# Optimization experiments

Measured on AMD Instinct MI355X. Metric: run time of the kernel, lower is better.

## Reference

```python
import jax, jax.numpy as jnp
import numpy as np

D = 128
N_ATOMS = 200000
E_ATOMS = 800000
G = 2000            # num molecule graphs = nDrug + nProtein
N_BIG = 7000        # nDrug + nProtein + nSe
E_BIG = 200000
N_EMB = 100001


def _edges(key, n, e):
    # random edges guaranteed to have no self-loops (PyG convs strip/re-add them)
    k1, k2 = jax.random.split(key)
    src = jax.random.randint(k1, (e,), 0, n)
    off = jax.random.randint(k2, (e,), 1, n)
    return jnp.stack([src, (src + off) % n])


def setup_inputs() -> dict:
    key = jax.random.key(0)
    ks = jax.random.split(key, 40)
    s = 0.09  # ~1/sqrt(D) init scale
    nrm = lambda i, shape: jax.random.normal(ks[i], shape, dtype=jnp.float32) * s
    inp = {}
    inp['x_ids'] = jax.random.randint(ks[0], (N_BIG,), 0, N_EMB)
    inp['drugEdges'] = _edges(ks[1], N_BIG, E_BIG)
    inp['seEdges'] = _edges(ks[2], 5000, 1000)  # unused by forward
    inp['drugNodes'] = jax.random.randint(ks[3], (1000,), 0, N_BIG)
    inp['seNodes'] = jax.random.randint(ks[4], (5000,), 0, N_BIG)
    inp['proteinNodes'] = jax.random.randint(ks[5], (1000,), 0, N_EMB)
    inp['proteinWeight'] = jax.random.normal(ks[6], (1000,), dtype=jnp.float32)
    inp['atom_x'] = jax.random.randint(ks[7], (N_ATOMS,), 0, N_EMB)
    inp['atom_edge_index'] = _edges(ks[8], N_ATOMS, E_ATOMS)
    inp['atom_batch'] = jnp.sort(jax.random.randint(ks[9], (N_ATOMS,), 0, G))
    inp['nDrug'] = 1000
    inp['emb'] = jax.random.uniform(ks[10], (N_EMB, D), minval=0.001, maxval=0.3, dtype=jnp.float32)
    for i in range(3):
        inp[f'gatW{i+1}'] = nrm(11 + i, (D, D))
        inp[f'attS{i+1}'] = nrm(14 + i, (D,))
        inp[f'attD{i+1}'] = nrm(17 + i, (D,))
        inp[f'gatB{i+1}'] = nrm(20 + i, (D,))
        inp[f'poolP{i+1}'] = nrm(23 + i, (D,))
    inp['lin1_W'] = nrm(26, (2 * D, D))
    inp['lin1_b'] = nrm(27, (D,))
    inp['gcn1_W'] = nrm(28, (D, D))
    inp['gcn1_b'] = nrm(29, (D,))
    inp['gcn2_W'] = nrm(30, (D, D))
    inp['gcn2_b'] = nrm(31, (D,))
    return inp


def _gat(x, src, dst, n, W, a_s, a_d, b):
    # PyG GATConv, 1 head: h = xW; e_ij = LeakyReLU(a_s.h_j + a_d.h_i);
    # softmax over incoming edges of i (self-loops re-added); out_i = sum_j alpha_ij h_j + b
    h = x @ W
    loops = jnp.arange(n)
    s = jnp.concatenate([src, loops])
    d = jnp.concatenate([dst, loops])
    e = jax.nn.leaky_relu((h @ a_s)[s] + (h @ a_d)[d], 0.2)
    m = jax.ops.segment_max(e, d, num_segments=n)
    ex = jnp.exp(e - m[d])
    z = jax.ops.segment_sum(ex, d, num_segments=n)
    w = ex / z[d]
    return jax.ops.segment_sum(w[:, None] * h[s], d, num_segments=n) + b


def _gcn(x, src, dst, n, W, b):
    loops = jnp.arange(n)
    s = jnp.concatenate([src, loops])
    d = jnp.concatenate([dst, loops])
    deg = jax.ops.segment_sum(jnp.ones(d.shape[0], x.dtype), d, num_segments=n)
    dis = deg ** -0.5
    coef = dis[s] * dis[d]
    return jax.ops.segment_sum(coef[:, None] * (x @ W)[s], d, num_segments=n) + b


def _topk1(x, p):
    # TopKPooling with ratio=1: keep all nodes, gate by tanh of projection score
    score = (x @ p) / jnp.linalg.norm(p)
    return x * jnp.tanh(score)[:, None]


def _gmp_gap(x, batch, g):
    mx = jax.ops.segment_max(x, batch, num_segments=g)
    sm = jax.ops.segment_sum(x, batch, num_segments=g)
    cnt = jax.ops.segment_sum(jnp.ones((x.shape[0], 1), x.dtype), batch, num_segments=g)
    return jnp.concatenate([mx, sm / jnp.maximum(cnt, 1.0)], axis=1)


def reference(x_ids, drugEdges, seEdges, drugNodes, seNodes, proteinNodes, proteinWeight,
              atom_x, atom_edge_index, atom_batch, nDrug, emb,
              gatW1, attS1, attD1, gatB1, poolP1,
              gatW2, attS2, attD2, gatB2, poolP2,
              gatW3, attS3, attD3, gatB3, poolP3,
              lin1_W, lin1_b, gcn1_W, gcn1_b, gcn2_W, gcn2_b):
    na = atom_x.shape[0]
    asrc, adst = atom_edge_index[0], atom_edge_index[1]
    xa = emb[atom_x]                                   # [na, D]
    xa = jax.nn.relu(_gat(xa, asrc, adst, na, gatW1, attS1, attD1, gatB1))
    xa = _topk1(xa, poolP1)
    x1 = _gmp_gap(xa, atom_batch, G)                   # [G, 2D]
    xa = jax.nn.relu(_gat(xa, asrc, adst, na, gatW2, attS2, attD2, gatB2))
    xa = _topk1(xa, poolP2)
    x2 = _gmp_gap(xa, atom_batch, G)
    xa = jax.nn.relu(_gat(xa, asrc, adst, na, gatW3, attS3, attD3, gatB3))
    xa = _topk1(xa, poolP3)
    x3 = _gmp_gap(xa, atom_batch, G)
    xDP = jax.nn.relu((x1 + x2 + x3) @ lin1_W + lin1_b)  # [G, D]
    nProtein = proteinNodes.shape[0]
    xse = emb[x_ids[nDrug + nProtein:]]                # side-effect node embeddings
    xb = jnp.concatenate([xDP, xse], axis=0)           # [N_BIG, D]
    dsrc, ddst = drugEdges[0], drugEdges[1]
    xb = jax.nn.relu(_gcn(xb, dsrc, ddst, N_BIG, gcn1_W, gcn1_b))
    xb = jax.nn.relu(_gcn(xb, dsrc, ddst, N_BIG, gcn2_W, gcn2_b))
    return (xb[drugNodes], xb[seNodes], xb)
```

## Files before the change

kernel.cpp:

```cpp
#include <hip/hip_runtime.h>
#include <cfloat>
#include <cmath>

#define D 128
#define N_ATOMS 200000
#define E_ATOMS 800000
#define G_GROUPS 2000
#define N_BIG 7000
#define E_BIG 200000
#define N_ALL (N_ATOMS + N_BIG)
#define E_ALL (E_ATOMS + E_BIG)

static inline int ceil_div(int a, int b) { return (a + b - 1) / b; }

typedef __attribute__((ext_vector_type(8))) short bf16x8;
typedef __attribute__((ext_vector_type(4))) float f32x4;

__device__ inline short f2bf(float f) {
  unsigned u = __builtin_bit_cast(unsigned, f);
  u = (u + 0x7FFF + ((u >> 16) & 1)) >> 16;
  return (short)u;
}
__device__ inline float bf2f(short h) {
  unsigned u = ((unsigned)(unsigned short)h) << 16;
  return __builtin_bit_cast(float, u);
}
__device__ inline float bflo(unsigned p) { return __builtin_bit_cast(float, p << 16); }
__device__ inline float bfhi(unsigned p) { return __builtin_bit_cast(float, p & 0xFFFF0000u); }
__device__ inline unsigned bfpack(float x, float y) {
  return ((unsigned)(unsigned short)f2bf(x)) | (((unsigned)(unsigned short)f2bf(y)) << 16);
}
__device__ inline float leaky(float e) { return fmaxf(e, 0.2f * e); }
__device__ inline float fast_tanh(float x) {
  float cx = fminf(fmaxf(x, -15.f), 15.f);
  float t = __expf(2.f * cx);
  return (t - 1.f) * __frcp_rn(t + 1.f);
}

__global__ void count_all(const int* __restrict__ adst, const int* __restrict__ ddst, int* __restrict__ deg,
                          int* __restrict__ rank) {
  int i = blockIdx.x * 256 + threadIdx.x;
  if (i < E_ATOMS)
    rank[i] = atomicAdd(&deg[adst[i]], 1);
  else if (i < E_ALL)
    rank[i] = atomicAdd(&deg[N_ATOMS + ddst[i - E_ATOMS]], 1);
}

__global__ void fill_csx(const int* __restrict__ asrc, const int* __restrict__ adst,
                         const int* __restrict__ dsrc, const int* __restrict__ ddst,
                         const int* __restrict__ rpx, const int* __restrict__ rank, int* __restrict__ csx) {
  int i = blockIdx.x * 256 + threadIdx.x;
  if (i < E_ATOMS) {
    csx[rpx[adst[i]] + rank[i]] = asrc[i];
  } else if (i < E_ALL) {
    int k = i - E_ATOMS;
    csx[rpx[N_ATOMS + ddst[k]] + rank[i]] = dsrc[k];
  }
}

__global__ void fill_pad(const int* __restrict__ deg, const int* __restrict__ rpx, int* __restrict__ csx) {
  int d = blockIdx.x * 256 + threadIdx.x;
  if (d >= N_ALL) return;
  int dg = deg[d];
  int b = rpx[d], e = rpx[d + 1];
  int sv = (d < N_ATOMS) ? d : d - N_ATOMS;
  for (int j = b + dg; j < e; ++j) csx[j] = sv;
}

__global__ void make_cntp(const int* __restrict__ deg, int* __restrict__ cntp, int n) {
  int i = blockIdx.x * 256 + threadIdx.x;
  if (i < n) cntp[i] = (deg[i] + 8) & ~7;
}

__global__ __launch_bounds__(256) void scan_phase1(const int* __restrict__ in, int* __restrict__ out,
                                                   int* __restrict__ bsums, int n) {
  __shared__ int lds[256];
  int t = threadIdx.x;
  int base = blockIdx.x * 1024;
  int v[4];
  int s = 0;
#pragma unroll
  for (int j = 0; j < 4; ++j) {
    int i = base + t * 4 + j;
    v[j] = (i < n) ? in[i] : 0;
    s += v[j];
  }
  lds[t] = s;
  __syncthreads();
  for (int off = 1; off < 256; off <<= 1) {
    int x = (t >= off) ? lds[t - off] : 0;
    __syncthreads();
    lds[t] += x;
    __syncthreads();
  }
  int excl = lds[t] - s;
  if (t == 255) bsums[blockIdx.x] = lds[255];
  int run = excl;
#pragma unroll
  for (int j = 0; j < 4; ++j) {
    int i = base + t * 4 + j;
    if (i < n) out[i] = run;
    run += v[j];
  }
}

__global__ __launch_bounds__(256) void scan_phase2(int* __restrict__ bsums, int* __restrict__ total_out, int nb) {
  __shared__ int lds[256];
  int t = threadIdx.x;
  int s = (t < nb) ? bsums[t] : 0;
  lds[t] = s;
  __syncthreads();
  for (int off = 1; off < 256; off <<= 1) {
    int x = (t >= off) ? lds[t - off] : 0;
    __syncthreads();
    lds[t] += x;
    __syncthreads();
  }
  if (t < nb) bsums[t] = lds[t] - s;
  if (t == 255) total_out[0] = lds[255];
}

__global__ void scan_phase3(int* __restrict__ out, const int* __restrict__ bsums, int n) {
  int i = blockIdx.x * 256 + threadIdx.x;
  if (i < n) out[i] += bsums[i >> 10];
}

__global__ __launch_bounds__(256) void prep_kernel(const float* __restrict__ W0, const float* __restrict__ W1,
                                                   const float* __restrict__ W2, const float* __restrict__ W3,
                                                   const float* __restrict__ W4, short* __restrict__ Wsplit,
                                                   const float* __restrict__ p0, const float* __restrict__ p1,
                                                   const float* __restrict__ p2, float* __restrict__ pn) {
  int b = blockIdx.x;
  if (b < 5) {
    const float* W = (b == 0) ? W0 : (b == 1) ? W1 : (b == 2) ? W2 : (b == 3) ? W3 : W4;
    short* dstH = Wsplit + (size_t)b * 16384;
    int t = threadIdx.x;
    int col = t & 127;
    int half = t >> 7;
#pragma unroll
    for (int kg = 0; kg < 8; ++kg) {
      int k0 = kg * 16 + half * 8;
      short vh[8];
#pragma unroll
      for (int j = 0; j < 8; ++j) vh[j] = f2bf(W[(k0 + j) * 128 + col]);
      int byte_off = (col * 256 + k0 * 2) ^ ((col & 7) << 4);
      *(bf16x8*)((char*)dstH + byte_off) = *(bf16x8*)vh;
    }
  } else {
    int t = threadIdx.x;
    int g = t >> 6, lane = t & 63;
    if (g < 3) {
      const float* p = (g == 0) ? p0 : (g == 1) ? p1 : p2;
      float2 v = ((const float2*)p)[lane];
      float s = v.x * v.x + v.y * v.y;
#pragma unroll
      for (int off = 32; off; off >>= 1) s += __shfl_xor(s, off);
      if (lane == 0) pn[g] = 1.f / sqrtf(s);
    }
  }
}

__global__ __launch_bounds__(512) void gemm_bf16(const short* __restrict__ A, const short* __restrict__ Wsp,
                                                 short* __restrict__ H, float* __restrict__ hs,
                                                 float* __restrict__ hd, const float* __restrict__ aS,
                                                 const float* __restrict__ aD, int M) {
  __shared__ short Wl[16384];
  int t = threadIdx.x;
  {
    const uint4* src = (const uint4*)Wsp;
    uint4* dst = (uint4*)Wl;
#pragma unroll
    for (int i = 0; i < 4; ++i) dst[t + i * 512] = src[t + i * 512];
  }
  __syncthreads();
  int wave = t >> 6, lane = t & 63;
  int lr = lane & 15, lq = lane >> 4;
  int row0 = blockIdx.x * 256 + wave * 32;
  f32x4 acc[2][8];
#pragma unroll
  for (int rt = 0; rt < 2; ++rt)
#pragma unroll
    for (int ct = 0; ct < 8; ++ct) acc[rt][ct] = (f32x4){0.f, 0.f, 0.f, 0.f};

#pragma unroll
  for (int ks = 0; ks < 4; ++ks) {
    int k8 = ks * 32 + lq * 8;
    bf16x8 Af[2];
#pragma unroll
    for (int rt = 0; rt < 2; ++rt) {
      int row = row0 + rt * 16 + lr;
      if (row < M) {
        Af[rt] = *(const bf16x8*)(A + (size_t)row * D + k8);
      } else {
        Af[rt] = (bf16x8){0, 0, 0, 0, 0, 0, 0, 0};
      }
    }
#pragma unroll
    for (int ct = 0; ct < 8; ++ct) {
      int col = ct * 16 + lr;
      int byte_off = (col * 256 + k8 * 2) ^ ((col & 7) << 4);
      bf16x8 Bh = *(bf16x8*)((char*)Wl + byte_off);
#pragma unroll
      for (int rt = 0; rt < 2; ++rt)
        acc[rt][ct] = __builtin_amdgcn_mfma_f32_16x16x32_bf16(Af[rt], Bh, acc[rt][ct], 0, 0, 0);
    }
  }
#pragma unroll
  for (int rt = 0; rt < 2; ++rt)
#pragma unroll
    for (int ct = 0; ct < 8; ++ct) {
      int col = ct * 16 + lr;
#pragma unroll
      for (int i = 0; i < 4; ++i) {
        int row = row0 + rt * 16 + lq * 4 + i;
        if (row < M) H[(size_t)row * D + col] = f2bf(acc[rt][ct][i]);
      }
    }
  if (aS) {
    float sA[8], sD[8];
#pragma unroll
    for (int ct = 0; ct < 8; ++ct) {
      sA[ct] = aS[ct * 16 + lr];
      sD[ct] = aD[ct * 16 + lr];
    }
#pragma unroll
    for (int rt = 0; rt < 2; ++rt)
#pragma unroll
      for (int i = 0; i < 4; ++i) {
        float ps = 0.f, pd = 0.f;
#pragma unroll
        for (int ct = 0; ct < 8; ++ct) {
          ps = fmaf(acc[rt][ct][i], sA[ct], ps);
          pd = fmaf(acc[rt][ct][i], sD[ct], pd);
        }
#pragma unroll
        for (int off = 1; off < 16; off <<= 1) {
          ps += __shfl_xor(ps, off);
          pd += __shfl_xor(pd, off);
        }
        int row = row0 + rt * 16 + lq * 4 + i;
        if (lr == 0 && row < M) {
          hs[row] = ps;
          hd[row] = pd;
        }
      }
  }
}

__global__ void edge_weights(const float* __restrict__ hs, const float* __restrict__ hd,
                             const int* __restrict__ rpx, const int* __restrict__ deg,
                             const int* __restrict__ csx, float* __restrict__ wts,
                             float* __restrict__ invz, int N) {
  int d = blockIdx.x * 256 + threadIdx.x;
  if (d >= N) return;
  int b = rpx[d];
  int cnt = rpx[d + 1] - b;
  int dg = deg[d];
  float hdd = hd[d];
  float es = leaky(hs[d] + hdd);
  float m = es;
  for (int j = 0; j < dg; ++j) m = fmaxf(m, leaky(hs[csx[b + j]] + hdd));
  float z = 0.f;
  for (int j = 0; j < dg; ++j) {
    float w = __expf(leaky(hs[csx[b + j]] + hdd) - m);
    wts[b + j] = w;
    z += w;
  }
  float wself = __expf(es - m);
  wts[b + dg] = wself;
  z += wself;
  for (int j = dg + 1; j < cnt; ++j) wts[b + j] = 0.f;
  invz[d] = 1.f / z;
}

__global__ void gcn_weights(const int* __restrict__ rpx, const int* __restrict__ deg,
                            const int* __restrict__ csx, const float* __restrict__ dis,
                            float* __restrict__ wtsG, int N) {
  int dl = blockIdx.x * 256 + threadIdx.x;
  if (dl >= N) return;
  int d = N_ATOMS + dl;
  int b = rpx[d];
  int cnt = rpx[d + 1] - b;
  int dg = deg[d];
  float dd = dis[dl];
  for (int j = 0; j < dg; ++j) wtsG[b + j] = dis[csx[b + j]] * dd;
  wtsG[b + dg] = dd * dd;
  for (int j = dg + 1; j < cnt; ++j) wtsG[b + j] = 0.f;
}

__global__ __launch_bounds__(256) void gat_gather(const short* __restrict__ H, const int* __restrict__ rpx,
                                                  const int* __restrict__ csx, const float* __restrict__ wts,
                                                  const float* __restrict__ invz, const float* __restrict__ bias,
                                                  const float* __restrict__ poolP, const float* __restrict__ pnL,
                                                  short* __restrict__ Xout, int N) {
  int wid = (blockIdx.x * 256 + threadIdx.x) >> 6;
  int d = __builtin_amdgcn_readfirstlane(wid);
  if (d >= N) return;
  int lane = threadIdx.x & 63;
  int rb = rpx[d];
  int cnt = rpx[d + 1] - rb;
  const unsigned* H2 = (const unsigned*)H;
  float ax = 0.f, ay = 0.f;
  for (int i = 0; i < cnt; i += 8) {
    int s0 = csx[rb + i + 0], s1 = csx[rb + i + 1], s2 = csx[rb + i + 2], s3 = csx[rb + i + 3];
    int s4 = csx[rb + i + 4], s5 = csx[rb + i + 5], s6 = csx[rb + i + 6], s7 = csx[rb + i + 7];
    float w0 = wts[rb + i + 0], w1 = wts[rb + i + 1], w2 = wts[rb + i + 2], w3 = wts[rb + i + 3];
    float w4 = wts[rb + i + 4], w5 = wts[rb + i + 5], w6 = wts[rb + i + 6], w7 = wts[rb + i + 7];
    unsigned h0 = H2[(size_t)s0 * 64 + lane];
    unsigned h1 = H2[(size_t)s1 * 64 + lane];
    unsigned h2 = H2[(size_t)s2 * 64 + lane];
    unsigned h3 = H2[(size_t)s3 * 64 + lane];
    unsigned h4 = H2[(size_t)s4 * 64 + lane];
    unsigned h5 = H2[(size_t)s5 * 64 + lane];
    unsigned h6 = H2[(size_t)s6 * 64 + lane];
    unsigned h7 = H2[(size_t)s7 * 64 + lane];
    ax = fmaf(w0, bflo(h0), ax);
    ay = fmaf(w0, bfhi(h0), ay);
    ax = fmaf(w1, bflo(h1), ax);
    ay = fmaf(w1, bfhi(h1), ay);
    ax = fmaf(w2, bflo(h2), ax);
    ay = fmaf(w2, bfhi(h2), ay);
    ax = fmaf(w3, bflo(h3), ax);
    ay = fmaf(w3, bfhi(h3), ay);
    ax = fmaf(w4, bflo(h4), ax);
    ay = fmaf(w4, bfhi(h4), ay);
    ax = fmaf(w5, bflo(h5), ax);
    ay = fmaf(w5, bfhi(h5), ay);
    ax = fmaf(w6, bflo(h6), ax);
    ay = fmaf(w6, bfhi(h6), ay);
    ax = fmaf(w7, bflo(h7), ax);
    ay = fmaf(w7, bfhi(h7), ay);
  }
  float iz = invz[d];
  float2 b2 = ((const float2*)bias)[lane];
  ax = fmaxf(fmaf(ax, iz, b2.x), 0.f);
  ay = fmaxf(fmaf(ay, iz, b2.y), 0.f);
  float2 p2 = ((const float2*)poolP)[lane];
  float dot = ax * p2.x + ay * p2.y;
#pragma unroll
  for (int off = 32; off; off >>= 1) dot += __shfl_xor(dot, off);
  float sc = fast_tanh(dot * pnL[0]);
  ((unsigned*)Xout)[(size_t)d * 64 + lane] = bfpack(ax * sc, ay * sc);
}

__global__ __launch_bounds__(256) void gcn_gather(const short* __restrict__ Y, const int* __restrict__ rpx,
                                                  const int* __restrict__ csx, const float* __restrict__ wtsG,
                                                  const float* __restrict__ b, short* __restrict__ outB,
                                                  float* __restrict__ outF, int N) {
  int wid = (blockIdx.x * 256 + threadIdx.x) >> 6;
  int dl = __builtin_amdgcn_readfirstlane(wid);
  if (dl >= N) return;
  int lane = threadIdx.x & 63;
  int rb = rpx[N_ATOMS + dl];
  int cnt = rpx[N_ATOMS + dl + 1] - rb;
  const unsigned* Y2 = (const unsigned*)Y;
  float ax = 0.f, ay = 0.f;
  for (int i = 0; i < cnt; i += 8) {
    int s0 = csx[rb + i + 0], s1 = csx[rb + i + 1], s2 = csx[rb + i + 2], s3 = csx[rb + i + 3];
    int s4 = csx[rb + i + 4], s5 = csx[rb + i + 5], s6 = csx[rb + i + 6], s7 = csx[rb + i + 7];
    float w0 = wtsG[rb + i + 0], w1 = wtsG[rb + i + 1], w2 = wtsG[rb + i + 2], w3 = wtsG[rb + i + 3];
    float w4 = wtsG[rb + i + 4], w5 = wtsG[rb + i + 5], w6 = wtsG[rb + i + 6], w7 = wtsG[rb + i + 7];
    unsigned h0 = Y2[(size_t)s0 * 64 + lane];
    unsigned h1 = Y2[(size_t)s1 * 64 + lane];
    unsigned h2 = Y2[(size_t)s2 * 64 + lane];
    unsigned h3 = Y2[(size_t)s3 * 64 + lane];
    unsigned h4 = Y2[(size_t)s4 * 64 + lane];
    unsigned h5 = Y2[(size_t)s5 * 64 + lane];
    unsigned h6 = Y2[(size_t)s6 * 64 + lane];
    unsigned h7 = Y2[(size_t)s7 * 64 + lane];
    ax = fmaf(w0, bflo(h0), ax);
    ay = fmaf(w0, bfhi(h0), ay);
    ax = fmaf(w1, bflo(h1), ax);
    ay = fmaf(w1, bfhi(h1), ay);
    ax = fmaf(w2, bflo(h2), ax);
    ay = fmaf(w2, bfhi(h2), ay);
    ax = fmaf(w3, bflo(h3), ax);
    ay = fmaf(w3, bfhi(h3), ay);
    ax = fmaf(w4, bflo(h4), ax);
    ay = fmaf(w4, bfhi(h4), ay);
    ax = fmaf(w5, bflo(h5), ax);
    ay = fmaf(w5, bfhi(h5), ay);
    ax = fmaf(w6, bflo(h6), ax);
    ay = fmaf(w6, bfhi(h6), ay);
    ax = fmaf(w7, bflo(h7), ax);
    ay = fmaf(w7, bfhi(h7), ay);
  }
  float2 b2 = ((const float2*)b)[lane];
  float ox = fmaxf(ax + b2.x, 0.f);
  float oy = fmaxf(ay + b2.y, 0.f);
  if (outF)
    ((float2*)outF)[(size_t)dl * 64 + lane] = make_float2(ox, oy);
  else
    ((unsigned*)outB)[(size_t)dl * 64 + lane] = bfpack(ox, oy);
}

__global__ void group_bounds(const int* __restrict__ batch, int* __restrict__ gs, int* __restrict__ ge, int n) {
  int i = blockIdx.x * 256 + threadIdx.x;
  if (i >= n) return;
  int b = batch[i];
  if (i == 0 || batch[i - 1] != b) gs[b] = i;
  if (i == n - 1 || batch[i + 1] != b) ge[b] = i + 1;
}

__global__ __launch_bounds__(256) void pool_kernel(const short* __restrict__ X, const int* __restrict__ gs,
                                                   const int* __restrict__ ge, float* __restrict__ x123) {
  __shared__ float2 mxs[4][64];
  __shared__ float2 sms[4][64];
  int g = blockIdx.x;
  int wv = threadIdx.x >> 6;
  int p = threadIdx.x & 63;
  int beg = gs[g], end = ge[g];
  int cnt = end - beg;
  const unsigned* X2 = (const unsigned*)X;
  float mx0 = -FLT_MAX, mx1 = -FLT_MAX, sm0 = 0.f, sm1 = 0.f;
  for (int i = beg + wv; i < end; i += 4) {
    unsigned v = X2[(size_t)i * 64 + p];
    float a = bflo(v), b = bfhi(v);
    mx0 = fmaxf(mx0, a);
    mx1 = fmaxf(mx1, b);
    sm0 += a;
    sm1 += b;
  }
  mxs[wv][p] = make_float2(mx0, mx1);
  sms[wv][p] = make_float2(sm0, sm1);
  __syncthreads();
  if (threadIdx.x < 64 && cnt > 0) {
#pragma unroll
    for (int k = 1; k < 4; ++k) {
      float2 m2 = mxs[k][p], s2 = sms[k][p];
      mx0 = fmaxf(mx0, m2.x);
      mx1 = fmaxf(mx1, m2.y);
      sm0 += s2.x;
      sm1 += s2.y;
    }
    float inv = 1.f / (float)cnt;
    float* xg = x123 + (size_t)g * 256;
    xg[2 * p] += mx0;
    xg[2 * p + 1] += mx1;
    xg[128 + 2 * p] += sm0 * inv;
    xg[128 + 2 * p + 1] += sm1 * inv;
  }
}

__global__ __launch_bounds__(128) void lin1_kernel(const float* __restrict__ x123, const float* __restrict__ W,
                                                   const float* __restrict__ b, short* __restrict__ xb) {
  __shared__ float row[256];
  int g = blockIdx.x;
  int c = threadIdx.x;
  row[c] = x123[(size_t)g * 256 + c];
  row[c + 128] = x123[(size_t)g * 256 + 128 + c];
  __syncthreads();
  float acc = b[c];
#pragma unroll 8
  for (int k = 0; k < 256; ++k) acc = fmaf(row[k], W[k * 128 + c], acc);
  xb[(size_t)g * D + c] = f2bf(fmaxf(acc, 0.f));
}

__global__ void xse_kernel(const float* __restrict__ emb, const int* __restrict__ x_ids,
                           const int* __restrict__ nDrugPtr, int nProtein, short* __restrict__ xb) {
  int idx = blockIdx.x * 256 + threadIdx.x;
  int r = idx >> 6, lane = idx & 63;
  int off = nDrugPtr[0] + nProtein;
  int id = x_ids[off + r];
  float2 v = ((const float2*)(emb + (size_t)id * D))[lane];
  ((unsigned*)xb)[(size_t)(G_GROUPS + r) * 64 + lane] = bfpack(v.x, v.y);
}

__global__ void dis_kernel(const int* __restrict__ deg, float* __restrict__ dis, int n) {
  int i = blockIdx.x * 256 + threadIdx.x;
  if (i < n) dis[i] = 1.f / sqrtf((float)(deg[N_ATOMS + i] + 1));
}

__global__ void gather_emb(const float* __restrict__ emb, const int* __restrict__ ids, short* __restrict__ out,
                           int n) {
  int idx = blockIdx.x * 256 + threadIdx.x;
  int node = idx >> 5, lane = idx & 31;
  if (node >= n) return;
  float4 v = ((const float4*)(emb + (size_t)ids[node] * D))[lane];
  uint2 o;
  o.x = bfpack(v.x, v.y);
  o.y = bfpack(v.z, v.w);
  ((uint2*)out)[(size_t)node * 32 + lane] = o;
}

__global__ void out_gather(const float* __restrict__ xb, const int* __restrict__ dn, const int* __restrict__ sn,
                           float* __restrict__ out) {
  int idx = blockIdx.x * 256 + threadIdx.x;
  int r = idx >> 6, lane = idx & 63;
  int s = (r < 1000) ? dn[r] : (r < 6000) ? sn[r - 1000] : (r - 6000);
  ((float2*)out)[(size_t)idx] = ((const float2*)(xb + (size_t)s * D))[lane];
}

extern "C" void kernel_launch(void* const* d_in, const int* in_sizes, int n_in, void* d_out, int out_size,
                              void* d_ws, size_t ws_size, hipStream_t stream) {
  const int* x_ids = (const int*)d_in[0];
  const int* drugE = (const int*)d_in[1];
  const int* drugNodes = (const int*)d_in[3];
  const int* seNodes = (const int*)d_in[4];
  int nProtein = in_sizes[5];
  const int* atom_x = (const int*)d_in[7];
  const int* atomE = (const int*)d_in[8];
  const int* atom_batch = (const int*)d_in[9];
  const int* nDrugPtr = (const int*)d_in[10];
  const float* emb = (const float*)d_in[11];
  const float* gatW[3] = {(const float*)d_in[12], (const float*)d_in[17], (const float*)d_in[22]};
  const float* attS[3] = {(const float*)d_in[13], (const float*)d_in[18], (const float*)d_in[23]};
  const float* attD[3] = {(const float*)d_in[14], (const float*)d_in[19], (const float*)d_in[24]};
  const float* gatB[3] = {(const float*)d_in[15], (const float*)d_in[20], (const float*)d_in[25]};
  const float* poolP[3] = {(const float*)d_in[16], (const float*)d_in[21], (const float*)d_in[26]};
  const float* lin1_W = (const float*)d_in[27];
  const float* lin1_b = (const float*)d_in[28];
  const float* gcn1_W = (const float*)d_in[29];
  const float* gcn1_b = (const float*)d_in[30];
  const float* gcn2_W = (const float*)d_in[31];
  const float* gcn2_b = (const float*)d_in[32];
  float* out = (float*)d_out;
  (void)n_in; (void)out_size; (void)ws_size;

  const int MAXX = E_ALL + 8 * N_ALL;

  char* ws = (char*)d_ws;
  size_t off = 0;
  auto alloc = [&](size_t bytes) -> char* {
    char* p = ws + off;
    off += (bytes + 255) & ~(size_t)255;
    return p;
  };
  short* bufA = (short*)alloc((size_t)N_ATOMS * D * 2);
  short* bufB = (short*)alloc((size_t)N_ATOMS * D * 2);
  float* hs = (float*)alloc((size_t)N_ATOMS * 4);
  float* hd = (float*)alloc((size_t)N_ATOMS * 4);
  int* csx = (int*)alloc((size_t)MAXX * 4);
  float* wts = (float*)alloc((size_t)MAXX * 4);
  float* wtsG = (float*)alloc((size_t)MAXX * 4);
  int* rank = (int*)alloc((size_t)E_ALL * 4);
  float* invz = (float*)alloc((size_t)N_ATOMS * 4);
  float* x123 = (float*)alloc((size_t)G_GROUPS * 256 * 4);
  short* xb1 = (short*)alloc((size_t)N_BIG * D * 2);
  short* xb2 = (short*)alloc((size_t)N_BIG * D * 2);
  float* xbF = (float*)alloc((size_t)N_BIG * D * 4);
  short* Wsplit = (short*)alloc((size_t)5 * 16384 * 2);
  int* rpx = (int*)alloc((size_t)(N_ALL + 1) * 4);
  int* deg = (int*)alloc((size_t)N_ALL * 4);
  int* cntp = (int*)alloc((size_t)N_ALL * 4);
  float* disB = (float*)alloc((size_t)N_BIG * 4);
  int* gs = (int*)alloc((size_t)G_GROUPS * 4);
  int* ge = (int*)alloc((size_t)G_GROUPS * 4);
  int* bsums = (int*)alloc(256 * 4);
  float* pn = (float*)alloc(256);

  const int* asrc = atomE;
  const int* adst = atomE + E_ATOMS;
  const int* dsrc = drugE;
  const int* ddst = drugE + E_BIG;

  prep_kernel<<<6, 256, 0, stream>>>(gatW[0], gatW[1], gatW[2], gcn1_W, gcn2_W, Wsplit, poolP[0], poolP[1],
                                     poolP[2], pn);

  hipMemsetAsync(deg, 0, (size_t)N_ALL * 4, stream);
  count_all<<<ceil_div(E_ALL, 256), 256, 0, stream>>>(adst, ddst, deg, rank);
  make_cntp<<<ceil_div(N_ALL, 256), 256, 0, stream>>>(deg, cntp, N_ALL);
  scan_phase1<<<ceil_div(N_ALL, 1024), 256, 0, stream>>>(cntp, rpx, bsums, N_ALL);
  scan_phase2<<<1, 256, 0, stream>>>(bsums, rpx + N_ALL, ceil_div(N_ALL, 1024));
  scan_phase3<<<ceil_div(N_ALL, 256), 256, 0, stream>>>(rpx, bsums, N_ALL);
  dis_kernel<<<ceil_div(N_BIG, 256), 256, 0, stream>>>(deg, disB, N_BIG);
  fill_csx<<<ceil_div(E_ALL, 256), 256, 0, stream>>>(asrc, adst, dsrc, ddst, rpx, rank, csx);
  fill_pad<<<ceil_div(N_ALL, 256), 256, 0, stream>>>(deg, rpx, csx);
  gcn_weights<<<ceil_div(N_BIG, 256), 256, 0, stream>>>(rpx, deg, csx, disB, wtsG, N_BIG);

  hipMemsetAsync(gs, 0, (size_t)G_GROUPS * 4, stream);
  hipMemsetAsync(ge, 0, (size_t)G_GROUPS * 4, stream);
  group_bounds<<<ceil_div(N_ATOMS, 256), 256, 0, stream>>>(atom_batch, gs, ge, N_ATOMS);

  gather_emb<<<ceil_div(N_ATOMS * 32, 256), 256, 0, stream>>>(emb, atom_x, bufA, N_ATOMS);
  hipMemsetAsync(x123, 0, (size_t)G_GROUPS * 256 * 4, stream);

  for (int L = 0; L < 3; ++L) {
    gemm_bf16<<<ceil_div(N_ATOMS, 256), 512, 0, stream>>>(bufA, Wsplit + (size_t)L * 16384, bufB, hs, hd,
                                                          attS[L], attD[L], N_ATOMS);
    edge_weights<<<ceil_div(N_ATOMS, 256), 256, 0, stream>>>(hs, hd, rpx, deg, csx, wts, invz, N_ATOMS);
    gat_gather<<<N_ATOMS * 64 / 256, 256, 0, stream>>>(bufB, rpx, csx, wts, invz, gatB[L], poolP[L], pn + L,
                                                       bufA, N_ATOMS);
    pool_kernel<<<G_GROUPS, 256, 0, stream>>>(bufA, gs, ge, x123);
  }

  lin1_kernel<<<G_GROUPS, 128, 0, stream>>>(x123, lin1_W, lin1_b, xb1);
  xse_kernel<<<(N_BIG - G_GROUPS) * 64 / 256, 256, 0, stream>>>(emb, x_ids, nDrugPtr, nProtein, xb1);

  gemm_bf16<<<ceil_div(N_BIG, 256), 512, 0, stream>>>(xb1, Wsplit + (size_t)3 * 16384, bufB, nullptr, nullptr,
                                                      nullptr, nullptr, N_BIG);
  gcn_gather<<<N_BIG * 64 / 256, 256, 0, stream>>>(bufB, rpx, csx, wtsG, gcn1_b, xb2, nullptr, N_BIG);
  gemm_bf16<<<ceil_div(N_BIG, 256), 512, 0, stream>>>(xb2, Wsplit + (size_t)4 * 16384, bufB, nullptr, nullptr,
                                                      nullptr, nullptr, N_BIG);
  gcn_gather<<<N_BIG * 64 / 256, 256, 0, stream>>>(bufB, rpx, csx, wtsG, gcn2_b, nullptr, xbF, N_BIG);

  out_gather<<<13000 * 64 / 256, 256, 0, stream>>>(xbF, drugNodes, seNodes, out);
}
```

Before: 526.8 us.

## Switch intermediate storage and gathers from bf16 to fp16 with packed half math

Replaces bf16 storage of activations and weights with fp16 and uses the fp16 MFMA in the GEMM. Edge weights are stored as duplicated half2 values, so the gather kernels can accumulate eight neighbours with packed half multiply-adds before one widening to float32, cutting VALU work in the gather loops. edge_weights also caches the leaky logits in the weight buffer so the second pass no longer regathers hs. The risks are fp16 range and precision: unnormalised softmax weights and partial sums are now accumulated in half precision. There is also a leftover no-op fmaf16 line in gat_gather.

```diff
diff --git a/kernel.cpp b/kernel.cpp
--- a/kernel.cpp
+++ b/kernel.cpp
@@ -13,22 +13,17 @@
 
 static inline int ceil_div(int a, int b) { return (a + b - 1) / b; }
 
-typedef __attribute__((ext_vector_type(8))) short bf16x8;
+typedef __attribute__((ext_vector_type(8))) _Float16 f16x8;
+typedef __attribute__((ext_vector_type(2))) _Float16 h2_t;
 typedef __attribute__((ext_vector_type(4))) float f32x4;
 
-__device__ inline short f2bf(float f) {
-  unsigned u = __builtin_bit_cast(unsigned, f);
-  u = (u + 0x7FFF + ((u >> 16) & 1)) >> 16;
-  return (short)u;
-}
-__device__ inline float bf2f(short h) {
-  unsigned u = ((unsigned)(unsigned short)h) << 16;
-  return __builtin_bit_cast(float, u);
-}
-__device__ inline float bflo(unsigned p) { return __builtin_bit_cast(float, p << 16); }
-__device__ inline float bfhi(unsigned p) { return __builtin_bit_cast(float, p & 0xFFFF0000u); }
-__device__ inline unsigned bfpack(float x, float y) {
-  return ((unsigned)(unsigned short)f2bf(x)) | (((unsigned)(unsigned short)f2bf(y)) << 16);
+__device__ inline h2_t u2h(unsigned u) { return __builtin_bit_cast(h2_t, u); }
+__device__ inline unsigned h2u(h2_t h) { return __builtin_bit_cast(unsigned, h); }
+__device__ inline unsigned packh2(float x, float y) {
+  h2_t h;
+  h[0] = (_Float16)x;
+  h[1] = (_Float16)y;
+  return h2u(h);
 }
 __device__ inline float leaky(float e) { return fmaxf(e, 0.2f * e); }
 __device__ inline float fast_tanh(float x) {
@@ -127,24 +122,24 @@
 
 __global__ __launch_bounds__(256) void prep_kernel(const float* __restrict__ W0, const float* __restrict__ W1,
                                                    const float* __restrict__ W2, const float* __restrict__ W3,
-                                                   const float* __restrict__ W4, short* __restrict__ Wsplit,
+                                                   const float* __restrict__ W4, unsigned short* __restrict__ Wsplit,
                                                    const float* __restrict__ p0, const float* __restrict__ p1,
                                                    const float* __restrict__ p2, float* __restrict__ pn) {
   int b = blockIdx.x;
   if (b < 5) {
     const float* W = (b == 0) ? W0 : (b == 1) ? W1 : (b == 2) ? W2 : (b == 3) ? W3 : W4;
-    short* dstH = Wsplit + (size_t)b * 16384;
+    unsigned short* dstH = Wsplit + (size_t)b * 16384;
     int t = threadIdx.x;
     int col = t & 127;
     int half = t >> 7;
 #pragma unroll
     for (int kg = 0; kg < 8; ++kg) {
       int k0 = kg * 16 + half * 8;
-      short vh[8];
-#pragma unroll
-      for (int j = 0; j < 8; ++j) vh[j] = f2bf(W[(k0 + j) * 128 + col]);
+      f16x8 vh;
+#pragma unroll
+      for (int j = 0; j < 8; ++j) vh[j] = (_Float16)W[(k0 + j) * 128 + col];
       int byte_off = (col * 256 + k0 * 2) ^ ((col & 7) << 4);
-      *(bf16x8*)((char*)dstH + byte_off) = *(bf16x8*)vh;
+      *(f16x8*)((char*)dstH + byte_off) = vh;
     }
   } else {
     int t = threadIdx.x;
@@ -160,11 +155,12 @@
   }
 }
 
-__global__ __launch_bounds__(512) void gemm_bf16(const short* __restrict__ A, const short* __restrict__ Wsp,
-                                                 short* __restrict__ H, float* __restrict__ hs,
-                                                 float* __restrict__ hd, const float* __restrict__ aS,
-                                                 const float* __restrict__ aD, int M) {
-  __shared__ short Wl[16384];
+__global__ __launch_bounds__(512) void gemm_f16(const unsigned short* __restrict__ A,
+                                                const unsigned short* __restrict__ Wsp,
+                                                unsigned short* __restrict__ H, float* __restrict__ hs,
+                                                float* __restrict__ hd, const float* __restrict__ aS,
+                                                const float* __restrict__ aD, int M) {
+  __shared__ unsigned short Wl[16384];
   int t = threadIdx.x;
   {
     const uint4* src = (const uint4*)Wsp;
@@ -185,24 +181,24 @@
 #pragma unroll
   for (int ks = 0; ks < 4; ++ks) {
     int k8 = ks * 32 + lq * 8;
-    bf16x8 Af[2];
+    f16x8 Af[2];
 #pragma unroll
     for (int rt = 0; rt < 2; ++rt) {
       int row = row0 + rt * 16 + lr;
       if (row < M) {
-        Af[rt] = *(const bf16x8*)(A + (size_t)row * D + k8);
+        Af[rt] = *(const f16x8*)(A + (size_t)row * D + k8);
       } else {
-        Af[rt] = (bf16x8){0, 0, 0, 0, 0, 0, 0, 0};
+        Af[rt] = (f16x8){0, 0, 0, 0, 0, 0, 0, 0};
       }
     }
 #pragma unroll
     for (int ct = 0; ct < 8; ++ct) {
       int col = ct * 16 + lr;
       int byte_off = (col * 256 + k8 * 2) ^ ((col & 7) << 4);
-      bf16x8 Bh = *(bf16x8*)((char*)Wl + byte_off);
+      f16x8 Bh = *(f16x8*)((char*)Wl + byte_off);
 #pragma unroll
       for (int rt = 0; rt < 2; ++rt)
-        acc[rt][ct] = __builtin_amdgcn_mfma_f32_16x16x32_bf16(Af[rt], Bh, acc[rt][ct], 0, 0, 0);
+        acc[rt][ct] = __builtin_amdgcn_mfma_f32_16x16x32_f16(Af[rt], Bh, acc[rt][ct], 0, 0, 0);
     }
   }
 #pragma unroll
@@ -213,7 +209,10 @@
 #pragma unroll
       for (int i = 0; i < 4; ++i) {
         int row = row0 + rt * 16 + lq * 4 + i;
-        if (row < M) H[(size_t)row * D + col] = f2bf(acc[rt][ct][i]);
+        if (row < M) {
+          _Float16 hv = (_Float16)acc[rt][ct][i];
+          H[(size_t)row * D + col] = __builtin_bit_cast(unsigned short, hv);
+        }
       }
     }
   if (aS) {
@@ -249,7 +248,7 @@
 
 __global__ void edge_weights(const float* __restrict__ hs, const float* __restrict__ hd,
                              const int* __restrict__ rpx, const int* __restrict__ deg,
-                             const int* __restrict__ csx, float* __restrict__ wts,
+                             const int* __restrict__ csx, unsigned* __restrict__ wts,
                              float* __restrict__ invz, int N) {
   int d = blockIdx.x * 256 + threadIdx.x;
   if (d >= N) return;
@@ -259,23 +258,28 @@
   float hdd = hd[d];
   float es = leaky(hs[d] + hdd);
   float m = es;
-  for (int j = 0; j < dg; ++j) m = fmaxf(m, leaky(hs[csx[b + j]] + hdd));
+  float* wf = (float*)wts;
+  for (int j = 0; j < dg; ++j) {
+    float e = leaky(hs[csx[b + j]] + hdd);
+    wf[b + j] = e;
+    m = fmaxf(m, e);
+  }
   float z = 0.f;
   for (int j = 0; j < dg; ++j) {
-    float w = __expf(leaky(hs[csx[b + j]] + hdd) - m);
-    wts[b + j] = w;
+    float w = __expf(wf[b + j] - m);
     z += w;
+    wts[b + j] = packh2(w, w);
   }
   float wself = __expf(es - m);
-  wts[b + dg] = wself;
+  wts[b + dg] = packh2(wself, wself);
   z += wself;
-  for (int j = dg + 1; j < cnt; ++j) wts[b + j] = 0.f;
+  for (int j = dg + 1; j < cnt; ++j) wts[b + j] = 0;
   invz[d] = 1.f / z;
 }
 
 __global__ void gcn_weights(const int* __restrict__ rpx, const int* __restrict__ deg,
                             const int* __restrict__ csx, const float* __restrict__ dis,
-                            float* __restrict__ wtsG, int N) {
+                            unsigned* __restrict__ wtsG, int N) {
   int dl = blockIdx.x * 256 + threadIdx.x;
   if (dl >= N) return;
   int d = N_ATOMS + dl;
@@ -283,16 +287,20 @@
   int cnt = rpx[d + 1] - b;
   int dg = deg[d];
   float dd = dis[dl];
-  for (int j = 0; j < dg; ++j) wtsG[b + j] = dis[csx[b + j]] * dd;
-  wtsG[b + dg] = dd * dd;
-  for (int j = dg + 1; j < cnt; ++j) wtsG[b + j] = 0.f;
-}
-
-__global__ __launch_bounds__(256) void gat_gather(const short* __restrict__ H, const int* __restrict__ rpx,
-                                                  const int* __restrict__ csx, const float* __restrict__ wts,
+  for (int j = 0; j < dg; ++j) {
+    float w = dis[csx[b + j]] * dd;
+    wtsG[b + j] = packh2(w, w);
+  }
+  wtsG[b + dg] = packh2(dd * dd, dd * dd);
+  for (int j = dg + 1; j < cnt; ++j) wtsG[b + j] = 0;
+}
+
+__global__ __launch_bounds__(256) void gat_gather(const unsigned short* __restrict__ H,
+                                                  const int* __restrict__ rpx, const int* __restrict__ csx,
+                                                  const unsigned* __restrict__ wts,
                                                   const float* __restrict__ invz, const float* __restrict__ bias,
                                                   const float* __restrict__ poolP, const float* __restrict__ pnL,
-                                                  short* __restrict__ Xout, int N) {
+                                                  unsigned short* __restrict__ Xout, int N) {
   int wid = (blockIdx.x * 256 + threadIdx.x) >> 6;
   int d = __builtin_amdgcn_readfirstlane(wid);
   if (d >= N) return;
@@ -304,8 +312,8 @@
   for (int i = 0; i < cnt; i += 8) {
     int s0 = csx[rb + i + 0], s1 = csx[rb + i + 1], s2 = csx[rb + i + 2], s3 = csx[rb + i + 3];
     int s4 = csx[rb + i + 4], s5 = csx[rb + i + 5], s6 = csx[rb + i + 6], s7 = csx[rb + i + 7];
-    float w0 = wts[rb + i + 0], w1 = wts[rb + i + 1], w2 = wts[rb + i + 2], w3 = wts[rb + i + 3];
-    float w4 = wts[rb + i + 4], w5 = wts[rb + i + 5], w6 = wts[rb + i + 6], w7 = wts[rb + i + 7];
+    unsigned w0 = wts[rb + i + 0], w1 = wts[rb + i + 1], w2 = wts[rb + i + 2], w3 = wts[rb + i + 3];
+    unsigned w4 = wts[rb + i + 4], w5 = wts[rb + i + 5], w6 = wts[rb + i + 6], w7 = wts[rb + i + 7];
     unsigned h0 = H2[(size_t)s0 * 64 + lane];
     unsigned h1 = H2[(size_t)s1 * 64 + lane];
     unsigned h2 = H2[(size_t)s2 * 64 + lane];
@@ -314,22 +322,18 @@
     unsigned h5 = H2[(size_t)s5 * 64 + lane];
     unsigned h6 = H2[(size_t)s6 * 64 + lane];
     unsigned h7 = H2[(size_t)s7 * 64 + lane];
-    ax = fmaf(w0, bflo(h0), ax);
-    ay = fmaf(w0, bfhi(h0), ay);
-    ax = fmaf(w1, bflo(h1), ax);
-    ay = fmaf(w1, bfhi(h1), ay);
-    ax = fmaf(w2, bflo(h2), ax);
-    ay = fmaf(w2, bfhi(h2), ay);
-    ax = fmaf(w3, bflo(h3), ax);
-    ay = fmaf(w3, bfhi(h3), ay);
-    ax = fmaf(w4, bflo(h4), ax);
-    ay = fmaf(w4, bfhi(h4), ay);
-    ax = fmaf(w5, bflo(h5), ax);
-    ay = fmaf(w5, bfhi(h5), ay);
-    ax = fmaf(w6, bflo(h6), ax);
-    ay = fmaf(w6, bfhi(h6), ay);
-    ax = fmaf(w7, bflo(h7), ax);
-    ay = fmaf(w7, bfhi(h7), ay);
+    h2_t a2 = u2h(w0) * u2h(h0);
+    a2 = __builtin_fmaf16(u2h(w1)[0], u2h(h1)[0], a2[0]) == a2[0] ? a2 : a2;
+    a2 += u2h(w1) * u2h(h1);
+    a2 += u2h(w2) * u2h(h2);
+    a2 += u2h(w3) * u2h(h3);
+    h2_t b2h = u2h(w4) * u2h(h4);
+    b2h += u2h(w5) * u2h(h5);
+    b2h += u2h(w6) * u2h(h6);
+    b2h += u2h(w7) * u2h(h7);
+    a2 += b2h;
+    ax += (float)a2[0];
+    ay += (float)a2[1];
   }
   float iz = invz[d];
   float2 b2 = ((const float2*)bias)[lane];
@@ -340,13 +344,14 @@
 #pragma unroll
   for (int off = 32; off; off >>= 1) dot += __shfl_xor(dot, off);
   float sc = fast_tanh(dot * pnL[0]);
-  ((unsigned*)Xout)[(size_t)d * 64 + lane] = bfpack(ax * sc, ay * sc);
-}
-
-__global__ __launch_bounds__(256) void gcn_gather(const short* __restrict__ Y, const int* __restrict__ rpx,
-                                                  const int* __restrict__ csx, const float* __restrict__ wtsG,
-                                                  const float* __restrict__ b, short* __restrict__ outB,
-                                                  float* __restrict__ outF, int N) {
+  ((unsigned*)Xout)[(size_t)d * 64 + lane] = packh2(ax * sc, ay * sc);
+}
+
+__global__ __launch_bounds__(256) void gcn_gather(const unsigned short* __restrict__ Y,
+                                                  const int* __restrict__ rpx, const int* __restrict__ csx,
+                                                  const unsigned* __restrict__ wtsG, const float* __restrict__ b,
+                                                  unsigned short* __restrict__ outB, float* __restrict__ outF,
+                                                  int N) {
   int wid = (blockIdx.x * 256 + threadIdx.x) >> 6;
   int dl = __builtin_amdgcn_readfirstlane(wid);
   if (dl >= N) return;
@@ -358,8 +363,8 @@
   for (int i = 0; i < cnt; i += 8) {
     int s0 = csx[rb + i + 0], s1 = csx[rb + i + 1], s2 = csx[rb + i + 2], s3 = csx[rb + i + 3];
     int s4 = csx[rb + i + 4], s5 = csx[rb + i + 5], s6 = csx[rb + i + 6], s7 = csx[rb + i + 7];
-    float w0 = wtsG[rb + i + 0], w1 = wtsG[rb + i + 1], w2 = wtsG[rb + i + 2], w3 = wtsG[rb + i + 3];
-    float w4 = wtsG[rb + i + 4], w5 = wtsG[rb + i + 5], w6 = wtsG[rb + i + 6], w7 = wtsG[rb + i + 7];
+    unsigned w0 = wtsG[rb + i + 0], w1 = wtsG[rb + i + 1], w2 = wtsG[rb + i + 2], w3 = wtsG[rb + i + 3];
+    unsigned w4 = wtsG[rb + i + 4], w5 = wtsG[rb + i + 5], w6 = wtsG[rb + i + 6], w7 = wtsG[rb + i + 7];
     unsigned h0 = Y2[(size_t)s0 * 64 + lane];
     unsigned h1 = Y2[(size_t)s1 * 64 + lane];
     unsigned h2 = Y2[(size_t)s2 * 64 + lane];
@@ -368,22 +373,17 @@
     unsigned h5 = Y2[(size_t)s5 * 64 + lane];
     unsigned h6 = Y2[(size_t)s6 * 64 + lane];
     unsigned h7 = Y2[(size_t)s7 * 64 + lane];
-    ax = fmaf(w0, bflo(h0), ax);
-    ay = fmaf(w0, bfhi(h0), ay);
-    ax = fmaf(w1, bflo(h1), ax);
-    ay = fmaf(w1, bfhi(h1), ay);
-    ax = fmaf(w2, bflo(h2), ax);
-    ay = fmaf(w2, bfhi(h2), ay);
-    ax = fmaf(w3, bflo(h3), ax);
-    ay = fmaf(w3, bfhi(h3), ay);
-    ax = fmaf(w4, bflo(h4), ax);
-    ay = fmaf(w4, bfhi(h4), ay);
-    ax = fmaf(w5, bflo(h5), ax);
-    ay = fmaf(w5, bfhi(h5), ay);
-    ax = fmaf(w6, bflo(h6), ax);
-    ay = fmaf(w6, bfhi(h6), ay);
-    ax = fmaf(w7, bflo(h7), ax);
-    ay = fmaf(w7, bfhi(h7), ay);
+    h2_t a2 = u2h(w0) * u2h(h0);
+    a2 += u2h(w1) * u2h(h1);
+    a2 += u2h(w2) * u2h(h2);
+    a2 += u2h(w3) * u2h(h3);
+    h2_t b2h = u2h(w4) * u2h(h4);
+    b2h += u2h(w5) * u2h(h5);
+    b2h += u2h(w6) * u2h(h6);
+    b2h += u2h(w7) * u2h(h7);
+    a2 += b2h;
+    ax += (float)a2[0];
+    ay += (float)a2[1];
   }
   float2 b2 = ((const float2*)b)[lane];
   float ox = fmaxf(ax + b2.x, 0.f);
@@ -391,7 +391,7 @@
   if (outF)
     ((float2*)outF)[(size_t)dl * 64 + lane] = make_float2(ox, oy);
   else
-    ((unsigned*)outB)[(size_t)dl * 64 + lane] = bfpack(ox, oy);
+    ((unsigned*)outB)[(size_t)dl * 64 + lane] = packh2(ox, oy);
 }
 
 __global__ void group_bounds(const int* __restrict__ batch, int* __restrict__ gs, int* __restrict__ ge, int n) {
@@ -402,8 +402,9 @@
   if (i == n - 1 || batch[i + 1] != b) ge[b] = i + 1;
 }
 
-__global__ __launch_bounds__(256) void pool_kernel(const short* __restrict__ X, const int* __restrict__ gs,
-                                                   const int* __restrict__ ge, float* __restrict__ x123) {
+__global__ __launch_bounds__(256) void pool_kernel(const unsigned short* __restrict__ X,
+                                                   const int* __restrict__ gs, const int* __restrict__ ge,
+                                                   float* __restrict__ x123) {
   __shared__ float2 mxs[4][64];
   __shared__ float2 sms[4][64];
   int g = blockIdx.x;
@@ -414,8 +415,8 @@
   const unsigned* X2 = (const unsigned*)X;
   float mx0 = -FLT_MAX, mx1 = -FLT_MAX, sm0 = 0.f, sm1 = 0.f;
   for (int i = beg + wv; i < end; i += 4) {
-    unsigned v = X2[(size_t)i * 64 + p];
-    float a = bflo(v), b = bfhi(v);
+    h2_t v = u2h(X2[(size_t)i * 64 + p]);
+    float a = (float)v[0], b = (float)v[1];
     mx0 = fmaxf(mx0, a);
     mx1 = fmaxf(mx1, b);
     sm0 += a;
@@ -443,7 +444,7 @@
 }
 
 __global__ __launch_bounds__(128) void lin1_kernel(const float* __restrict__ x123, const float* __restrict__ W,
-                                                   const float* __restrict__ b, short* __restrict__ xb) {
+                                                   const float* __restrict__ b, unsigned short* __restrict__ xb) {
   __shared__ float row[256];
   int g = blockIdx.x;
   int c = threadIdx.x;
@@ -453,17 +454,18 @@
   float acc = b[c];
 #pragma unroll 8
   for (int k = 0; k < 256; ++k) acc = fmaf(row[k], W[k * 128 + c], acc);
-  xb[(size_t)g * D + c] = f2bf(fmaxf(acc, 0.f));
+  _Float16 hv = (_Float16)fmaxf(acc, 0.f);
+  xb[(size_t)g * D + c] = __builtin_bit_cast(unsigned short, hv);
 }
 
 __global__ void xse_kernel(const float* __restrict__ emb, const int* __restrict__ x_ids,
-                           const int* __restrict__ nDrugPtr, int nProtein, short* __restrict__ xb) {
+                           const int* __restrict__ nDrugPtr, int nProtein, unsigned short* __restrict__ xb) {
   int idx = blockIdx.x * 256 + threadIdx.x;
   int r = idx >> 6, lane = idx & 63;
   int off = nDrugPtr[0] + nProtein;
   int id = x_ids[off + r];
   float2 v = ((const float2*)(emb + (size_t)id * D))[lane];
-  ((unsigned*)xb)[(size_t)(G_GROUPS + r) * 64 + lane] = bfpack(v.x, v.y);
+  ((unsigned*)xb)[(size_t)(G_GROUPS + r) * 64 + lane] = packh2(v.x, v.y);
 }
 
 __global__ void dis_kernel(const int* __restrict__ deg, float* __restrict__ dis, int n) {
@@ -471,15 +473,15 @@
   if (i < n) dis[i] = 1.f / sqrtf((float)(deg[N_ATOMS + i] + 1));
 }
 
-__global__ void gather_emb(const float* __restrict__ emb, const int* __restrict__ ids, short* __restrict__ out,
-                           int n) {
+__global__ void gather_emb(const float* __restrict__ emb, const int* __restrict__ ids,
+                           unsigned short* __restrict__ out, int n) {
   int idx = blockIdx.x * 256 + threadIdx.x;
   int node = idx >> 5, lane = idx & 31;
   if (node >= n) return;
   float4 v = ((const float4*)(emb + (size_t)ids[node] * D))[lane];
   uint2 o;
-  o.x = bfpack(v.x, v.y);
-  o.y = bfpack(v.z, v.w);
+  o.x = packh2(v.x, v.y);
+  o.y = packh2(v.z, v.w);
   ((uint2*)out)[(size_t)node * 32 + lane] = o;
 }
 
@@ -526,20 +528,20 @@
     off += (bytes + 255) & ~(size_t)255;
     return p;
   };
-  short* bufA = (short*)alloc((size_t)N_ATOMS * D * 2);
-  short* bufB = (short*)alloc((size_t)N_ATOMS * D * 2);
+  unsigned short* bufA = (unsigned short*)alloc((size_t)N_ATOMS * D * 2);
+  unsigned short* bufB = (unsigned short*)alloc((size_t)N_ATOMS * D * 2);
   float* hs = (float*)alloc((size_t)N_ATOMS * 4);
   float* hd = (float*)alloc((size_t)N_ATOMS * 4);
   int* csx = (int*)alloc((size_t)MAXX * 4);
-  float* wts = (float*)alloc((size_t)MAXX * 4);
-  float* wtsG = (float*)alloc((size_t)MAXX * 4);
+  unsigned* wts = (unsigned*)alloc((size_t)MAXX * 4);
+  unsigned* wtsG = (unsigned*)alloc((size_t)MAXX * 4);
   int* rank = (int*)alloc((size_t)E_ALL * 4);
   float* invz = (float*)alloc((size_t)N_ATOMS * 4);
   float* x123 = (float*)alloc((size_t)G_GROUPS * 256 * 4);
-  short* xb1 = (short*)alloc((size_t)N_BIG * D * 2);
-  short* xb2 = (short*)alloc((size_t)N_BIG * D * 2);
+  unsigned short* xb1 = (unsigned short*)alloc((size_t)N_BIG * D * 2);
+  unsigned short* xb2 = (unsigned short*)alloc((size_t)N_BIG * D * 2);
   float* xbF = (float*)alloc((size_t)N_BIG * D * 4);
-  short* Wsplit = (short*)alloc((size_t)5 * 16384 * 2);
+  unsigned short* Wsplit = (unsigned short*)alloc((size_t)5 * 16384 * 2);
   int* rpx = (int*)alloc((size_t)(N_ALL + 1) * 4);
   int* deg = (int*)alloc((size_t)N_ALL * 4);
   int* cntp = (int*)alloc((size_t)N_ALL * 4);
@@ -576,8 +578,8 @@
   hipMemsetAsync(x123, 0, (size_t)G_GROUPS * 256 * 4, stream);
 
   for (int L = 0; L < 3; ++L) {
-    gemm_bf16<<<ceil_div(N_ATOMS, 256), 512, 0, stream>>>(bufA, Wsplit + (size_t)L * 16384, bufB, hs, hd,
-                                                          attS[L], attD[L], N_ATOMS);
+    gemm_f16<<<ceil_div(N_ATOMS, 256), 512, 0, stream>>>(bufA, Wsplit + (size_t)L * 16384, bufB, hs, hd,
+                                                         attS[L], attD[L], N_ATOMS);
     edge_weights<<<ceil_div(N_ATOMS, 256), 256, 0, stream>>>(hs, hd, rpx, deg, csx, wts, invz, N_ATOMS);
     gat_gather<<<N_ATOMS * 64 / 256, 256, 0, stream>>>(bufB, rpx, csx, wts, invz, gatB[L], poolP[L], pn + L,
                                                        bufA, N_ATOMS);
@@ -587,11 +589,11 @@
   lin1_kernel<<<G_GROUPS, 128, 0, stream>>>(x123, lin1_W, lin1_b, xb1);
   xse_kernel<<<(N_BIG - G_GROUPS) * 64 / 256, 256, 0, stream>>>(emb, x_ids, nDrugPtr, nProtein, xb1);
 
-  gemm_bf16<<<ceil_div(N_BIG, 256), 512, 0, stream>>>(xb1, Wsplit + (size_t)3 * 16384, bufB, nullptr, nullptr,
-                                                      nullptr, nullptr, N_BIG);
+  gemm_f16<<<ceil_div(N_BIG, 256), 512, 0, stream>>>(xb1, Wsplit + (size_t)3 * 16384, bufB, nullptr, nullptr,
+                                                     nullptr, nullptr, N_BIG);
   gcn_gather<<<N_BIG * 64 / 256, 256, 0, stream>>>(bufB, rpx, csx, wtsG, gcn1_b, xb2, nullptr, N_BIG);
-  gemm_bf16<<<ceil_div(N_BIG, 256), 512, 0, stream>>>(xb2, Wsplit + (size_t)4 * 16384, bufB, nullptr, nullptr,
-                                                      nullptr, nullptr, N_BIG);
+  gemm_f16<<<ceil_div(N_BIG, 256), 512, 0, stream>>>(xb2, Wsplit + (size_t)4 * 16384, bufB, nullptr, nullptr,
+                                                     nullptr, nullptr, N_BIG);
   gcn_gather<<<N_BIG * 64 / 256, 256, 0, stream>>>(bufB, rpx, csx, wtsG, gcn2_b, nullptr, xbF, N_BIG);
 
   out_gather<<<13000 * 64 / 256, 256, 0, stream>>>(xbF, drugNodes, seNodes, out);
```

After: 526.8 us. No clear change (-0.0%).
